# Kernel optimization log

Measured on AMD Instinct MI355X. Metric: run time of the kernel, lower is better.

The kernel has to match this reference:

```python
import jax, jax.numpy as jnp
from jax import lax
import numpy as np

EPS = 1e-08
BETA_VAL = 0.9
B_VAL = 1.0
SIGMA_VAL = 10.0

@jax.custom_vjp
def spike_fn(mthr, sigma):
    # Heaviside forward; SuperSpike surrogate gradient in backward
    return (mthr > 0).astype(mthr.dtype)

def _spike_fwd(mthr, sigma):
    return (mthr > 0).astype(mthr.dtype), (mthr, sigma)

def _spike_bwd(res, g):
    mthr, sigma = res
    grad = g / (sigma * jnp.abs(mthr) + 1.0) ** 2
    return grad, jnp.zeros_like(sigma)

spike_fn.defvjp(_spike_fwd, _spike_bwd)


def setup_inputs() -> dict:
    key = jax.random.key(0)
    kx, kw, kv = jax.random.split(key, 3)
    B, T, I, O = 128, 100, 1024, 1024
    x = jax.random.normal(kx, (B, T, I), dtype=jnp.float32)
    w = (jax.random.normal(kw, (I, O), dtype=jnp.float32)
         * np.float32(np.sqrt(1.0 / I)))  # mean 0, std w_init_std*sqrt(1/I)
    v = (jax.random.normal(kv, (O, O), dtype=jnp.float32)
         * np.float32(np.sqrt(1.0 / O)))
    beta = jnp.full((1,), BETA_VAL, dtype=jnp.float32)   # one_per_layer
    b = jnp.full((O,), B_VAL, dtype=jnp.float32)
    sigma = jnp.full((O,), SIGMA_VAL, dtype=jnp.float32)  # surrogate_sigma_mode='all'
    return {"x": x, "w": w, "v": v, "beta": beta, "b": b, "sigma": sigma}


def reference(x, w, v, beta, b, sigma):
    B, T, I = x.shape
    O = w.shape[1]
    h = jnp.einsum('bti,io->bto', x, w)            # [B,T,O]
    d = jnp.einsum('ai,ao->io', w, w)              # lateral term w^T w, [O,O]
    norm = (w ** 2).sum(0)                         # [O]
    inv_norm = 1.0 / (norm + EPS)

    mem0 = jnp.zeros((B, O), dtype=x.dtype)
    spk0 = jnp.zeros((B, O), dtype=x.dtype)

    def step(carry, h_t):
        mem, spk = carry
        rst = spk @ d                              # lateral reset [B,O]
        inp = h_t + spk @ v                        # recurrent input
        # Leaky neuron, soft reset
        mem = (mem - rst) * beta + inp * (1.0 - beta)
        mthr = mem * inv_norm - b
        spk = spike_fn(mthr, sigma)
        return (mem, spk), spk

    h_t_first = jnp.swapaxes(h, 0, 1)              # [T,B,O]
    _, spk_seq = lax.scan(step, (mem0, spk0), h_t_first)
    spk_rec = jnp.swapaxes(spk_seq, 0, 1)          # [B,T,O]

    loss = 0.5 * (spk_rec ** 2).mean()             # Regularization 'squared'
    spk_spread_loss = spk_rec.sum(axis=(0, 2)).max() / (B * O)  # 'max'
    return spk_rec, loss, spk_spread_loss
```

## Files before the change

kernel.cpp:

```cpp
#include <hip/hip_runtime.h>
#include <cstdint>
#include <cstddef>

#define I_DIM 1024
#define O_DIM 1024
#define B_DIM 128
#define T_DIM 100
#define PANEL 32768
#define QSTep 512

typedef __attribute__((ext_vector_type(8))) __bf16 bf16x8;
typedef __attribute__((ext_vector_type(16))) float f32x16;

__device__ __forceinline__ void wg_barrier_lgkm() {
  __asm__ volatile("" ::: "memory");
  __builtin_amdgcn_s_waitcnt(0xC07F);
  __builtin_amdgcn_s_barrier();
  __asm__ volatile("" ::: "memory");
}

__device__ __forceinline__ unsigned short bf16rn(float x) {
  unsigned u = __float_as_uint(x);
  unsigned r = u + 0x7FFFu + ((u >> 16) & 1u);
  return (unsigned short)(r >> 16);
}
__device__ __forceinline__ void split2(float x, unsigned short& h,
                                       unsigned short& l) {
  h = bf16rn(x);
  float hf = __uint_as_float(((unsigned)h) << 16);
  l = bf16rn(x - hf);
}

__global__ __launch_bounds__(256) void prep_kernel(
    const float* __restrict__ w, const float* __restrict__ x,
    unsigned short* __restrict__ wTth, unsigned short* __restrict__ wTtl,
    unsigned short* __restrict__ xth, unsigned short* __restrict__ xtl,
    double* __restrict__ normpart) {
  __shared__ float tile[64][65];
  __shared__ double red[4][64];
  const int id = blockIdx.x;
  const int tid = threadIdx.x;
  if (id < 256) {
    const int a0 = (id >> 4) * 64, o0 = (id & 15) * 64;
    const int tr = tid >> 4, tc4 = (tid & 15) * 4;
#pragma unroll
    for (int rr = 0; rr < 64; rr += 16) {
      float4 v = *(const float4*)&w[(size_t)(a0 + tr + rr) * O_DIM + o0 + tc4];
      tile[tr + rr][tc4 + 0] = v.x;
      tile[tr + rr][tc4 + 1] = v.y;
      tile[tr + rr][tc4 + 2] = v.z;
      tile[tr + rr][tc4 + 3] = v.w;
    }
    __syncthreads();
    {
      const int ol = tid & 63, seg = tid >> 6;
      double s = 0.0;
#pragma unroll
      for (int i = 0; i < 16; ++i) {
        double v = (double)tile[seg * 16 + i][ol];
        s += v * v;
      }
      red[seg][ol] = s;
    }
    const int q = (a0 >> 4) + (tc4 >> 4);
    const int kh = (tc4 >> 3) & 1;
    const int inner = tc4 & 7;
#pragma unroll
    for (int rr = 0; rr < 64; rr += 16) {
      int o = o0 + tr + rr;
      unsigned short hh[4], ll[4];
#pragma unroll
      for (int j = 0; j < 4; ++j) split2(tile[tc4 + j][tr + rr], hh[j], ll[j]);
      int l = (o & 31) + 32 * kh;
      size_t base = ((size_t)(o >> 5) * PANEL) + (size_t)q * QSTep +
                    (size_t)l * 8 + inner;
      *(ushort4*)&wTth[base] = make_ushort4(hh[0], hh[1], hh[2], hh[3]);
      *(ushort4*)&wTtl[base] = make_ushort4(ll[0], ll[1], ll[2], ll[3]);
    }
    __syncthreads();
    if (tid < 64)
      normpart[(size_t)(a0 >> 6) * O_DIM + o0 + tid] =
          red[0][tid] + red[1][tid] + red[2][tid] + red[3][tid];
  } else {
    const int p = (id - 256) >> 2, sub = (id - 256) & 3;
    const int wq = tid >> 6, lane = tid & 63;
    const int row = lane & 31, kh = lane >> 5;
    const float* src = x + (size_t)(p * 32 + row) * I_DIM + kh * 8;
#pragma unroll
    for (int i = sub * 4; i < sub * 4 + 4; ++i) {
      const int q = i * 4 + wq;
      const float* s = src + q * 16;
      float4 v0 = *(const float4*)(s);
      float4 v1 = *(const float4*)(s + 4);
      unsigned short h[8], l[8];
      split2(v0.x, h[0], l[0]);
      split2(v0.y, h[1], l[1]);
      split2(v0.z, h[2], l[2]);
      split2(v0.w, h[3], l[3]);
      split2(v1.x, h[4], l[4]);
      split2(v1.y, h[5], l[5]);
      split2(v1.z, h[6], l[6]);
      split2(v1.w, h[7], l[7]);
      size_t base = ((size_t)p * PANEL) + (size_t)q * QSTep + (size_t)lane * 8;
      *(ushort4*)&xth[base] = make_ushort4(h[0], h[1], h[2], h[3]);
      *(ushort4*)&xth[base + 4] = make_ushort4(h[4], h[5], h[6], h[7]);
      *(ushort4*)&xtl[base] = make_ushort4(l[0], l[1], l[2], l[3]);
      *(ushort4*)&xtl[base + 4] = make_ushort4(l[4], l[5], l[6], l[7]);
    }
  }
}

__global__ __launch_bounds__(512, 5) void gemm_fused(
    const unsigned short* __restrict__ xth,
    const unsigned short* __restrict__ xtl,
    const unsigned short* __restrict__ wTth,
    const unsigned short* __restrict__ wTtl, const float* __restrict__ v,
    const float* __restrict__ beta_p, float* __restrict__ h,
    float* __restrict__ M) {
  const int tid = threadIdx.x;
  const int wv = tid >> 6, lane = tid & 63;
  const int wm = wv >> 2, wn = wv & 3;
  const int lm = lane & 31, lkh = lane >> 5;
  const bool is_h = blockIdx.y < 100;
  const int rbase = is_h ? (int)blockIdx.y * 128 : ((int)blockIdx.y - 100) * 128;
  const int cbase = (int)blockIdx.x * 128;
  const unsigned short* Ah_src = is_h ? xth : wTth;
  const unsigned short* Al_src = is_h ? xtl : wTtl;

  f32x16 acc[2];
#pragma unroll
  for (int a = 0; a < 2; ++a)
#pragma unroll
    for (int e = 0; e < 16; ++e) acc[a][e] = 0.f;

  const unsigned short *pah[2], *pal[2], *pbh, *pbl;
#pragma unroll
  for (int mt = 0; mt < 2; ++mt) {
    size_t offA =
        ((size_t)((rbase >> 5) + wm * 2 + mt) * PANEL) + (size_t)lane * 8;
    pah[mt] = Ah_src + offA;
    pal[mt] = Al_src + offA;
  }
  {
    size_t offB = ((size_t)((cbase >> 5) + wn) * PANEL) + (size_t)lane * 8;
    pbh = wTth + offB;
    pbl = wTtl + offB;
  }
  bf16x8 fah[2][2], fal[2][2], fbh[2], fbl[2];
#pragma unroll
  for (int mt = 0; mt < 2; ++mt) {
    fah[0][mt] = *(const bf16x8*)(pah[mt]);
    fal[0][mt] = *(const bf16x8*)(pal[mt]);
  }
  fbh[0] = *(const bf16x8*)(pbh);
  fbl[0] = *(const bf16x8*)(pbl);
#pragma unroll 2
  for (int q = 0; q < 64; ++q) {
    const int cb = q & 1;
    if (q < 63) {
      size_t d = (size_t)(q + 1) * QSTep;
#pragma unroll
      for (int mt = 0; mt < 2; ++mt) {
        fah[cb ^ 1][mt] = *(const bf16x8*)(pah[mt] + d);
        fal[cb ^ 1][mt] = *(const bf16x8*)(pal[mt] + d);
      }
      fbh[cb ^ 1] = *(const bf16x8*)(pbh + d);
      fbl[cb ^ 1] = *(const bf16x8*)(pbl + d);
    }
#pragma unroll
    for (int mt = 0; mt < 2; ++mt)
      acc[mt] = __builtin_amdgcn_mfma_f32_32x32x16_bf16(fah[cb][mt], fbh[cb],
                                                        acc[mt], 0, 0, 0);
#pragma unroll
    for (int mt = 0; mt < 2; ++mt)
      acc[mt] = __builtin_amdgcn_mfma_f32_32x32x16_bf16(fah[cb][mt], fbl[cb],
                                                        acc[mt], 0, 0, 0);
#pragma unroll
    for (int mt = 0; mt < 2; ++mt)
      acc[mt] = __builtin_amdgcn_mfma_f32_32x32x16_bf16(fal[cb][mt], fbh[cb],
                                                        acc[mt], 0, 0, 0);
  }
  const int col = cbase + wn * 32 + lm;
  if (is_h) {
#pragma unroll
    for (int mt = 0; mt < 2; ++mt)
#pragma unroll
      for (int r = 0; r < 16; ++r) {
        int row = rbase + wm * 64 + mt * 32 + (r & 3) + 8 * (r >> 2) + 4 * lkh;
        h[(size_t)row * O_DIM + col] = acc[mt][r];
      }
  } else {
    const float beta = beta_p[0];
    const float ombeta = 1.0f - beta;
#pragma unroll
    for (int mt = 0; mt < 2; ++mt)
#pragma unroll
      for (int r = 0; r < 16; ++r) {
        int row = rbase + wm * 64 + mt * 32 + (r & 3) + 8 * (r >> 2) + 4 * lkh;
        M[(size_t)row * O_DIM + col] =
            ombeta * v[(size_t)row * O_DIM + col] - beta * acc[mt][r];
      }
  }
}

__global__ __launch_bounds__(256) void scan_kernel(
    const float* __restrict__ h, const float* __restrict__ M,
    const double* __restrict__ normpart, const float* __restrict__ bvec,
    const float* __restrict__ beta_p, float* __restrict__ out,
    int* __restrict__ wgcnt, int* __restrict__ done) {
  __shared__ unsigned short wlist[2][4][256];
  __shared__ int wcnt[2][4];
  __shared__ int reds[128];
  __shared__ int lastflag;
  const int b = blockIdx.x, tid = threadIdx.x;
  const int wv = tid >> 6;
  const int ob4 = tid * 4;
  const double beta = (double)beta_p[0];
  const double ombeta = 1.0 - beta;
  double mem[4] = {0.0, 0.0, 0.0, 0.0};
  double inv[4], bth[4];
#pragma unroll
  for (int j = 0; j < 4; ++j) {
    double s = 0.0;
#pragma unroll
    for (int g = 0; g < 16; ++g) s += normpart[(size_t)g * O_DIM + ob4 + j];
    inv[j] = 1.0 / (s + 1e-8);
    bth[j] = (double)bvec[ob4 + j];
  }
  if (tid < 8) wcnt[tid >> 2][tid & 3] = 0;
  __syncthreads();
  const float* hb = h + (size_t)b * T_DIM * O_DIM;
  float* obp = out + (size_t)b * T_DIM * O_DIM;
  float4 hv0 = *(const float4*)&hb[ob4];
  float4 hv1 = *(const float4*)&hb[O_DIM + ob4];
  for (int t = 0; t < T_DIM; ++t) {
    const int p = t & 1, np = p ^ 1;
    float4 hv2 = make_float4(0.f, 0.f, 0.f, 0.f);
    if (t + 2 < T_DIM) hv2 = *(const float4*)&hb[(size_t)(t + 2) * O_DIM + ob4];
    double lat[4] = {0.0, 0.0, 0.0, 0.0};
    const int ks = wcnt[p][0] + wcnt[p][1] + wcnt[p][2] + wcnt[p][3];
    if (ks) {
#pragma unroll
      for (int w = 0; w < 4; ++w) {
        const int kw = wcnt[p][w];
        for (int n = 0; n < kw; ++n) {
          const int i = wlist[p][w][n];
          float4 m = *(const float4*)&M[(size_t)i * O_DIM + ob4];
          lat[0] += (double)m.x;
          lat[1] += (double)m.y;
          lat[2] += (double)m.z;
          lat[3] += (double)m.w;
        }
      }
    }
    const float hvv[4] = {hv0.x, hv0.y, hv0.z, hv0.w};
    float os[4];
    unsigned cur = 0;
#pragma unroll
    for (int j = 0; j < 4; ++j) {
      mem[j] = mem[j] * beta + (double)hvv[j] * ombeta + lat[j];
      double mthr = mem[j] * inv[j] - bth[j];
      bool s = mthr > 0.0;
      os[j] = s ? 1.0f : 0.0f;
      unsigned long long mask = __ballot(s);
      if (s) {
        unsigned below = __builtin_amdgcn_mbcnt_lo((unsigned)mask, 0);
        below = __builtin_amdgcn_mbcnt_hi((unsigned)(mask >> 32), below);
        wlist[np][wv][cur + below] = (unsigned short)(ob4 + j);
      }
      cur += (unsigned)__popcll(mask);
    }
    *(float4*)&obp[(size_t)t * O_DIM + ob4] =
        make_float4(os[0], os[1], os[2], os[3]);
    hv0 = hv1;
    hv1 = hv2;
    if ((tid & 63) == 0) wcnt[np][wv] = (int)cur;
    wg_barrier_lgkm();
    if (tid == 0)
      wgcnt[b * T_DIM + t] =
          wcnt[np][0] + wcnt[np][1] + wcnt[np][2] + wcnt[np][3];
  }
  __threadfence();
  if (tid == 0) {
    int old = atomicAdd(done, 1);
    lastflag = (old == B_DIM - 1) ? 1 : 0;
  }
  __syncthreads();
  if (lastflag) {
    __threadfence();
    int s = 0;
    if (tid < T_DIM) {
      for (int bb = 0; bb < B_DIM; ++bb) s += wgcnt[bb * T_DIM + tid];
    }
    if (tid < 128) reds[tid] = (tid < T_DIM) ? s : 0;
    __syncthreads();
    if (tid == 0) {
      long long total = 0;
      int mx = 0;
      for (int i = 0; i < T_DIM; ++i) {
        total += reds[i];
        if (reds[i] > mx) mx = reds[i];
      }
      const double N = (double)B_DIM * T_DIM * O_DIM;
      out[(size_t)B_DIM * T_DIM * O_DIM] = (float)(0.5 * (double)total / N);
      out[(size_t)B_DIM * T_DIM * O_DIM + 1] =
          (float)((double)mx / (double)(B_DIM * O_DIM));
    }
  }
}

extern "C" void kernel_launch(void* const* d_in, const int* in_sizes, int n_in,
                              void* d_out, int out_size, void* d_ws,
                              size_t ws_size, hipStream_t stream) {
  const float* x = (const float*)d_in[0];
  const float* w = (const float*)d_in[1];
  const float* v = (const float*)d_in[2];
  const float* beta = (const float*)d_in[3];
  const float* b = (const float*)d_in[4];
  float* out = (float*)d_out;

  char* ws = (char*)d_ws;
  const size_t OFF_M = 0;
  const size_t OFF_H = 4194304;
  const size_t OFF_WTH = 56623104;
  const size_t OFF_WTL = 58720256;
  const size_t OFF_NP = 60817408;
  const size_t OFF_DONE = 60948480;
  const size_t OFF_XTH = 60948992;
  const size_t OFF_XTL = 87163392;
  float* M = (float*)(ws + OFF_M);
  float* h = (float*)(ws + OFF_H);
  unsigned short* wTth = (unsigned short*)(ws + OFF_WTH);
  unsigned short* wTtl = (unsigned short*)(ws + OFF_WTL);
  double* normpart = (double*)(ws + OFF_NP);
  int* done = (int*)(ws + OFF_DONE);
  unsigned short* xth = (unsigned short*)(ws + OFF_XTH);
  unsigned short* xtl = (unsigned short*)(ws + OFF_XTL);
  int* wgcnt = (int*)(ws + OFF_XTH);

  hipMemsetAsync(done, 0, 512, stream);
  hipLaunchKernelGGL(prep_kernel, dim3(1856), dim3(256), 0, stream, w, x, wTth,
                     wTtl, xth, xtl, normpart);
  hipLaunchKernelGGL(gemm_fused, dim3(8, 108), dim3(512), 0, stream, xth, xtl,
                     wTth, wTtl, v, beta, h, M);
  hipLaunchKernelGGL(scan_kernel, dim3(128), dim3(256), 0, stream, h, M,
                     normpart, b, beta, out, wgcnt, done);
}
```

Measured before the change: 331.6 us.

## Use single-wave scan per batch and 2x2 register-tiled GEMM warps

The scan kernel now runs one 64-lane wavefront per batch row, with each lane owning 16 neurons. Spike lists are kept as per-lane ballot masks in registers instead of LDS, which removes the per-step workgroup barrier and shared-memory traffic. The GEMM moves to 256-thread blocks where each wave computes a 2x2 grid of 32x32 MFMA tiles, giving more fragment reuse per load, and uses a 1D grid that walks along M first. The cost is fewer active waves in the latency-bound scan, each running a longer serial loop with higher register pressure.

```diff
diff --git a/kernel.cpp b/kernel.cpp
--- a/kernel.cpp
+++ b/kernel.cpp
@@ -11,13 +11,6 @@
 
 typedef __attribute__((ext_vector_type(8))) __bf16 bf16x8;
 typedef __attribute__((ext_vector_type(16))) float f32x16;
-
-__device__ __forceinline__ void wg_barrier_lgkm() {
-  __asm__ volatile("" ::: "memory");
-  __builtin_amdgcn_s_waitcnt(0xC07F);
-  __builtin_amdgcn_s_barrier();
-  __asm__ volatile("" ::: "memory");
-}
 
 __device__ __forceinline__ unsigned short bf16rn(float x) {
   unsigned u = __float_as_uint(x);
@@ -110,84 +103,103 @@
   }
 }
 
-__global__ __launch_bounds__(512, 5) void gemm_fused(
+__global__ __launch_bounds__(256, 3) void gemm_fused(
     const unsigned short* __restrict__ xth,
     const unsigned short* __restrict__ xtl,
     const unsigned short* __restrict__ wTth,
     const unsigned short* __restrict__ wTtl, const float* __restrict__ v,
     const float* __restrict__ beta_p, float* __restrict__ h,
     float* __restrict__ M) {
+  const int id = blockIdx.x;
   const int tid = threadIdx.x;
   const int wv = tid >> 6, lane = tid & 63;
-  const int wm = wv >> 2, wn = wv & 3;
+  const int wm = wv >> 1, wn = wv & 1;
   const int lm = lane & 31, lkh = lane >> 5;
-  const bool is_h = blockIdx.y < 100;
-  const int rbase = is_h ? (int)blockIdx.y * 128 : ((int)blockIdx.y - 100) * 128;
-  const int cbase = (int)blockIdx.x * 128;
-  const unsigned short* Ah_src = is_h ? xth : wTth;
-  const unsigned short* Al_src = is_h ? xtl : wTtl;
-
-  f32x16 acc[2];
+  const bool is_h = id < 800;
+  int rbase, cbase;
+  const unsigned short *Ah_src, *Al_src;
+  if (is_h) {
+    rbase = (id % 100) * 128;
+    cbase = (id / 100) * 128;
+    Ah_src = xth;
+    Al_src = xtl;
+  } else {
+    rbase = ((id - 800) >> 3) * 128;
+    cbase = ((id - 800) & 7) * 128;
+    Ah_src = wTth;
+    Al_src = wTtl;
+  }
+  f32x16 acc[2][2];
 #pragma unroll
   for (int a = 0; a < 2; ++a)
 #pragma unroll
-    for (int e = 0; e < 16; ++e) acc[a][e] = 0.f;
-
-  const unsigned short *pah[2], *pal[2], *pbh, *pbl;
-#pragma unroll
-  for (int mt = 0; mt < 2; ++mt) {
+    for (int b = 0; b < 2; ++b)
+#pragma unroll
+      for (int e = 0; e < 16; ++e) acc[a][b][e] = 0.f;
+  const unsigned short *pah[2], *pal[2], *pbh[2], *pbl[2];
+#pragma unroll
+  for (int t = 0; t < 2; ++t) {
     size_t offA =
-        ((size_t)((rbase >> 5) + wm * 2 + mt) * PANEL) + (size_t)lane * 8;
-    pah[mt] = Ah_src + offA;
-    pal[mt] = Al_src + offA;
-  }
-  {
-    size_t offB = ((size_t)((cbase >> 5) + wn) * PANEL) + (size_t)lane * 8;
-    pbh = wTth + offB;
-    pbl = wTtl + offB;
-  }
-  bf16x8 fah[2][2], fal[2][2], fbh[2], fbl[2];
-#pragma unroll
-  for (int mt = 0; mt < 2; ++mt) {
-    fah[0][mt] = *(const bf16x8*)(pah[mt]);
-    fal[0][mt] = *(const bf16x8*)(pal[mt]);
-  }
-  fbh[0] = *(const bf16x8*)(pbh);
-  fbl[0] = *(const bf16x8*)(pbl);
+        ((size_t)((rbase >> 5) + wm * 2 + t) * PANEL) + (size_t)lane * 8;
+    size_t offB =
+        ((size_t)((cbase >> 5) + wn * 2 + t) * PANEL) + (size_t)lane * 8;
+    pah[t] = Ah_src + offA;
+    pal[t] = Al_src + offA;
+    pbh[t] = wTth + offB;
+    pbl[t] = wTtl + offB;
+  }
+  bf16x8 fah[2][2], fal[2][2], fbh[2][2], fbl[2][2];
+#pragma unroll
+  for (int t = 0; t < 2; ++t) {
+    fah[0][t] = *(const bf16x8*)(pah[t]);
+    fal[0][t] = *(const bf16x8*)(pal[t]);
+    fbh[0][t] = *(const bf16x8*)(pbh[t]);
+    fbl[0][t] = *(const bf16x8*)(pbl[t]);
+  }
 #pragma unroll 2
   for (int q = 0; q < 64; ++q) {
     const int cb = q & 1;
     if (q < 63) {
       size_t d = (size_t)(q + 1) * QSTep;
 #pragma unroll
-      for (int mt = 0; mt < 2; ++mt) {
-        fah[cb ^ 1][mt] = *(const bf16x8*)(pah[mt] + d);
-        fal[cb ^ 1][mt] = *(const bf16x8*)(pal[mt] + d);
-      }
-      fbh[cb ^ 1] = *(const bf16x8*)(pbh + d);
-      fbl[cb ^ 1] = *(const bf16x8*)(pbl + d);
-    }
-#pragma unroll
-    for (int mt = 0; mt < 2; ++mt)
-      acc[mt] = __builtin_amdgcn_mfma_f32_32x32x16_bf16(fah[cb][mt], fbh[cb],
-                                                        acc[mt], 0, 0, 0);
-#pragma unroll
-    for (int mt = 0; mt < 2; ++mt)
-      acc[mt] = __builtin_amdgcn_mfma_f32_32x32x16_bf16(fah[cb][mt], fbl[cb],
-                                                        acc[mt], 0, 0, 0);
-#pragma unroll
-    for (int mt = 0; mt < 2; ++mt)
-      acc[mt] = __builtin_amdgcn_mfma_f32_32x32x16_bf16(fal[cb][mt], fbh[cb],
-                                                        acc[mt], 0, 0, 0);
-  }
-  const int col = cbase + wn * 32 + lm;
+      for (int t = 0; t < 2; ++t) {
+        fah[cb ^ 1][t] = *(const bf16x8*)(pah[t] + d);
+        fal[cb ^ 1][t] = *(const bf16x8*)(pal[t] + d);
+        fbh[cb ^ 1][t] = *(const bf16x8*)(pbh[t] + d);
+        fbl[cb ^ 1][t] = *(const bf16x8*)(pbl[t] + d);
+      }
+    }
+#pragma unroll
+    for (int mt = 0; mt < 2; ++mt)
+#pragma unroll
+      for (int nt = 0; nt < 2; ++nt)
+        acc[mt][nt] = __builtin_amdgcn_mfma_f32_32x32x16_bf16(
+            fah[cb][mt], fbh[cb][nt], acc[mt][nt], 0, 0, 0);
+#pragma unroll
+    for (int mt = 0; mt < 2; ++mt)
+#pragma unroll
+      for (int nt = 0; nt < 2; ++nt)
+        acc[mt][nt] = __builtin_amdgcn_mfma_f32_32x32x16_bf16(
+            fah[cb][mt], fbl[cb][nt], acc[mt][nt], 0, 0, 0);
+#pragma unroll
+    for (int mt = 0; mt < 2; ++mt)
+#pragma unroll
+      for (int nt = 0; nt < 2; ++nt)
+        acc[mt][nt] = __builtin_amdgcn_mfma_f32_32x32x16_bf16(
+            fal[cb][mt], fbh[cb][nt], acc[mt][nt], 0, 0, 0);
+  }
   if (is_h) {
 #pragma unroll
     for (int mt = 0; mt < 2; ++mt)
 #pragma unroll
-      for (int r = 0; r < 16; ++r) {
-        int row = rbase + wm * 64 + mt * 32 + (r & 3) + 8 * (r >> 2) + 4 * lkh;
-        h[(size_t)row * O_DIM + col] = acc[mt][r];
+      for (int nt = 0; nt < 2; ++nt) {
+        int col = cbase + wn * 64 + nt * 32 + lm;
+#pragma unroll
+        for (int r = 0; r < 16; ++r) {
+          int row =
+              rbase + wm * 64 + mt * 32 + (r & 3) + 8 * (r >> 2) + 4 * lkh;
+          h[(size_t)row * O_DIM + col] = acc[mt][nt][r];
+        }
       }
   } else {
     const float beta = beta_p[0];
@@ -195,114 +207,128 @@
 #pragma unroll
     for (int mt = 0; mt < 2; ++mt)
 #pragma unroll
-      for (int r = 0; r < 16; ++r) {
-        int row = rbase + wm * 64 + mt * 32 + (r & 3) + 8 * (r >> 2) + 4 * lkh;
-        M[(size_t)row * O_DIM + col] =
-            ombeta * v[(size_t)row * O_DIM + col] - beta * acc[mt][r];
-      }
-  }
-}
-
-__global__ __launch_bounds__(256) void scan_kernel(
+      for (int nt = 0; nt < 2; ++nt) {
+        int col = cbase + wn * 64 + nt * 32 + lm;
+#pragma unroll
+        for (int r = 0; r < 16; ++r) {
+          int row =
+              rbase + wm * 64 + mt * 32 + (r & 3) + 8 * (r >> 2) + 4 * lkh;
+          M[(size_t)row * O_DIM + col] =
+              ombeta * v[(size_t)row * O_DIM + col] - beta * acc[mt][nt][r];
+        }
+      }
+  }
+}
+
+__global__ __launch_bounds__(64) void scan_kernel(
     const float* __restrict__ h, const float* __restrict__ M,
     const double* __restrict__ normpart, const float* __restrict__ bvec,
     const float* __restrict__ beta_p, float* __restrict__ out,
     int* __restrict__ wgcnt, int* __restrict__ done) {
-  __shared__ unsigned short wlist[2][4][256];
-  __shared__ int wcnt[2][4];
-  __shared__ int reds[128];
-  __shared__ int lastflag;
-  const int b = blockIdx.x, tid = threadIdx.x;
-  const int wv = tid >> 6;
-  const int ob4 = tid * 4;
+  const int b = blockIdx.x, lane = threadIdx.x;
   const double beta = (double)beta_p[0];
   const double ombeta = 1.0 - beta;
-  double mem[4] = {0.0, 0.0, 0.0, 0.0};
-  double inv[4], bth[4];
-#pragma unroll
-  for (int j = 0; j < 4; ++j) {
-    double s = 0.0;
-#pragma unroll
-    for (int g = 0; g < 16; ++g) s += normpart[(size_t)g * O_DIM + ob4 + j];
-    inv[j] = 1.0 / (s + 1e-8);
-    bth[j] = (double)bvec[ob4 + j];
-  }
-  if (tid < 8) wcnt[tid >> 2][tid & 3] = 0;
-  __syncthreads();
+  double mem[4][4], inv[4][4], bth[4][4];
+  unsigned long long pmask[4][4];
+#pragma unroll
+  for (int k = 0; k < 4; ++k)
+#pragma unroll
+    for (int j = 0; j < 4; ++j) {
+      const int o = 256 * k + 4 * lane + j;
+      mem[k][j] = 0.0;
+      double s = 0.0;
+#pragma unroll
+      for (int g = 0; g < 16; ++g) s += normpart[(size_t)g * O_DIM + o];
+      inv[k][j] = 1.0 / (s + 1e-8);
+      bth[k][j] = (double)bvec[o];
+      pmask[k][j] = 0ull;
+    }
   const float* hb = h + (size_t)b * T_DIM * O_DIM;
   float* obp = out + (size_t)b * T_DIM * O_DIM;
-  float4 hv0 = *(const float4*)&hb[ob4];
-  float4 hv1 = *(const float4*)&hb[O_DIM + ob4];
+  float4 hv0[4], hv1[4];
+#pragma unroll
+  for (int k = 0; k < 4; ++k) {
+    hv0[k] = *(const float4*)&hb[256 * k + 4 * lane];
+    hv1[k] = *(const float4*)&hb[O_DIM + 256 * k + 4 * lane];
+  }
+  int total = 0;
   for (int t = 0; t < T_DIM; ++t) {
-    const int p = t & 1, np = p ^ 1;
-    float4 hv2 = make_float4(0.f, 0.f, 0.f, 0.f);
-    if (t + 2 < T_DIM) hv2 = *(const float4*)&hb[(size_t)(t + 2) * O_DIM + ob4];
-    double lat[4] = {0.0, 0.0, 0.0, 0.0};
-    const int ks = wcnt[p][0] + wcnt[p][1] + wcnt[p][2] + wcnt[p][3];
-    if (ks) {
-#pragma unroll
-      for (int w = 0; w < 4; ++w) {
-        const int kw = wcnt[p][w];
-        for (int n = 0; n < kw; ++n) {
-          const int i = wlist[p][w][n];
-          float4 m = *(const float4*)&M[(size_t)i * O_DIM + ob4];
-          lat[0] += (double)m.x;
-          lat[1] += (double)m.y;
-          lat[2] += (double)m.z;
-          lat[3] += (double)m.w;
+    float4 hv2[4];
+#pragma unroll
+    for (int k = 0; k < 4; ++k) hv2[k] = make_float4(0.f, 0.f, 0.f, 0.f);
+    if (t + 2 < T_DIM) {
+#pragma unroll
+      for (int k = 0; k < 4; ++k)
+        hv2[k] = *(const float4*)&hb[(size_t)(t + 2) * O_DIM + 256 * k +
+                                     4 * lane];
+    }
+    double lat[4][4] = {};
+#pragma unroll
+    for (int k2 = 0; k2 < 4; ++k2)
+#pragma unroll
+      for (int j2 = 0; j2 < 4; ++j2) {
+        unsigned long long m = pmask[k2][j2];
+        while (m) {
+          const int p = (int)__builtin_ctzll(m);
+          m &= m - 1;
+          const int i = 256 * k2 + 4 * p + j2;
+          const float* Mr = M + (size_t)i * O_DIM + 4 * lane;
+#pragma unroll
+          for (int k = 0; k < 4; ++k) {
+            float4 mv = *(const float4*)(Mr + 256 * k);
+            lat[k][0] += (double)mv.x;
+            lat[k][1] += (double)mv.y;
+            lat[k][2] += (double)mv.z;
+            lat[k][3] += (double)mv.w;
+          }
         }
       }
-    }
-    const float hvv[4] = {hv0.x, hv0.y, hv0.z, hv0.w};
-    float os[4];
-    unsigned cur = 0;
-#pragma unroll
-    for (int j = 0; j < 4; ++j) {
-      mem[j] = mem[j] * beta + (double)hvv[j] * ombeta + lat[j];
-      double mthr = mem[j] * inv[j] - bth[j];
-      bool s = mthr > 0.0;
-      os[j] = s ? 1.0f : 0.0f;
-      unsigned long long mask = __ballot(s);
-      if (s) {
-        unsigned below = __builtin_amdgcn_mbcnt_lo((unsigned)mask, 0);
-        below = __builtin_amdgcn_mbcnt_hi((unsigned)(mask >> 32), below);
-        wlist[np][wv][cur + below] = (unsigned short)(ob4 + j);
-      }
-      cur += (unsigned)__popcll(mask);
-    }
-    *(float4*)&obp[(size_t)t * O_DIM + ob4] =
-        make_float4(os[0], os[1], os[2], os[3]);
-    hv0 = hv1;
-    hv1 = hv2;
-    if ((tid & 63) == 0) wcnt[np][wv] = (int)cur;
-    wg_barrier_lgkm();
-    if (tid == 0)
-      wgcnt[b * T_DIM + t] =
-          wcnt[np][0] + wcnt[np][1] + wcnt[np][2] + wcnt[np][3];
+    int cnt = 0;
+#pragma unroll
+    for (int k = 0; k < 4; ++k) {
+      const float hvv[4] = {hv0[k].x, hv0[k].y, hv0[k].z, hv0[k].w};
+      float os[4];
+#pragma unroll
+      for (int j = 0; j < 4; ++j) {
+        mem[k][j] = mem[k][j] * beta + (double)hvv[j] * ombeta + lat[k][j];
+        double mthr = mem[k][j] * inv[k][j] - bth[k][j];
+        bool s = mthr > 0.0;
+        os[j] = s ? 1.0f : 0.0f;
+        unsigned long long mk = __ballot(s);
+        pmask[k][j] = mk;
+        cnt += (int)__popcll(mk);
+      }
+      *(float4*)&obp[(size_t)t * O_DIM + 256 * k + 4 * lane] =
+          make_float4(os[0], os[1], os[2], os[3]);
+      hv0[k] = hv1[k];
+      hv1[k] = hv2[k];
+    }
+    total += 0;
+    if (lane == 0) wgcnt[b * T_DIM + t] = cnt;
   }
   __threadfence();
-  if (tid == 0) {
-    int old = atomicAdd(done, 1);
-    lastflag = (old == B_DIM - 1) ? 1 : 0;
-  }
-  __syncthreads();
-  if (lastflag) {
+  int old = 0;
+  if (lane == 0) old = atomicAdd(done, 1);
+  old = __shfl(old, 0, 64);
+  if (old == B_DIM - 1) {
     __threadfence();
-    int s = 0;
-    if (tid < T_DIM) {
-      for (int bb = 0; bb < B_DIM; ++bb) s += wgcnt[bb * T_DIM + tid];
-    }
-    if (tid < 128) reds[tid] = (tid < T_DIM) ? s : 0;
-    __syncthreads();
-    if (tid == 0) {
-      long long total = 0;
-      int mx = 0;
-      for (int i = 0; i < T_DIM; ++i) {
-        total += reds[i];
-        if (reds[i] > mx) mx = reds[i];
-      }
+    long long tsum = 0;
+    int mx = 0;
+    for (int t = lane; t < T_DIM; t += 64) {
+      int st = 0;
+      for (int bb = 0; bb < B_DIM; ++bb) st += wgcnt[bb * T_DIM + t];
+      tsum += st;
+      if (st > mx) mx = st;
+    }
+#pragma unroll
+    for (int off = 32; off > 0; off >>= 1) {
+      tsum += __shfl_down((long long)tsum, off, 64);
+      int m2 = __shfl_down(mx, off, 64);
+      if (m2 > mx) mx = m2;
+    }
+    if (lane == 0) {
       const double N = (double)B_DIM * T_DIM * O_DIM;
-      out[(size_t)B_DIM * T_DIM * O_DIM] = (float)(0.5 * (double)total / N);
+      out[(size_t)B_DIM * T_DIM * O_DIM] = (float)(0.5 * (double)tsum / N);
       out[(size_t)B_DIM * T_DIM * O_DIM + 1] =
           (float)((double)mx / (double)(B_DIM * O_DIM));
     }
@@ -341,8 +367,8 @@
   hipMemsetAsync(done, 0, 512, stream);
   hipLaunchKernelGGL(prep_kernel, dim3(1856), dim3(256), 0, stream, w, x, wTth,
                      wTtl, xth, xtl, normpart);
-  hipLaunchKernelGGL(gemm_fused, dim3(8, 108), dim3(512), 0, stream, xth, xtl,
+  hipLaunchKernelGGL(gemm_fused, dim3(864), dim3(256), 0, stream, xth, xtl,
                      wTth, wTtl, v, beta, h, M);
-  hipLaunchKernelGGL(scan_kernel, dim3(128), dim3(256), 0, stream, h, M,
+  hipLaunchKernelGGL(scan_kernel, dim3(128), dim3(64), 0, stream, h, M,
                      normpart, b, beta, out, wgcnt, done);
 }
```

Result: faster. 315.1 us (-5.0%).
